# Kernel optimization log

Hardware: AMD Instinct MI355X
Metric: run time of the kernel (lower is better)

Reference implementation:

```python
import jax, jax.numpy as jnp
import numpy as np

NUM_HEADS = 16

def setup_inputs() -> dict:
    key = jax.random.key(0)
    ks = jax.random.split(key, 5)
    B, T, C = 2, 2048, 1024
    s = 0.02
    return {
        "x": jax.random.normal(ks[0], (B, T, C), dtype=jnp.float32),
        "attn_w": jax.random.normal(ks[1], (3 * C, C), dtype=jnp.float32) * s,
        "attn_b": jax.random.normal(ks[2], (3 * C,), dtype=jnp.float32) * s,
        "proj_w": jax.random.normal(ks[3], (C, C), dtype=jnp.float32) * s,
        "proj_b": jax.random.normal(ks[4], (C,), dtype=jnp.float32) * s,
    }

def reference(x, attn_w, attn_b, proj_w, proj_b):
    B, T, C = x.shape
    H = NUM_HEADS
    D = C // H
    # fused QKV projection (torch Linear: x @ W^T + b)
    qkv = x @ attn_w.T + attn_b                      # [B, T, 3C]
    q, k, v = jnp.split(qkv, 3, axis=-1)             # each [B, T, C]
    # split heads -> [B, H, T, D]
    def heads(t):
        return t.reshape(B, T, H, D).transpose(0, 2, 1, 3)
    q, k, v = heads(q), heads(k), heads(v)
    scale = 1.0 / jnp.sqrt(jnp.asarray(D, dtype=x.dtype))
    scores = jnp.einsum("bhtd,bhsd->bhts", q, k) * scale   # [B, H, T, T]
    causal = jnp.tril(jnp.ones((T, T), dtype=bool))
    scores = jnp.where(causal[None, None], scores, jnp.asarray(-jnp.inf, dtype=scores.dtype))
    att = jax.nn.softmax(scores, axis=-1)
    out = jnp.einsum("bhts,bhsd->bhtd", att, v)      # [B, H, T, D]
    out = out.transpose(0, 2, 1, 3).reshape(B, T, C)
    return out @ proj_w.T + proj_b
```

## Files before the change

kernel.cpp:

```cpp
#include <hip/hip_runtime.h>
#include <hip/hip_bf16.h>

typedef __bf16 bf16_t;
typedef __bf16 bf16x4 __attribute__((ext_vector_type(4)));
typedef __bf16 bf16x8 __attribute__((ext_vector_type(8)));
typedef float f32x4 __attribute__((ext_vector_type(4)));
typedef float f32x8 __attribute__((ext_vector_type(8)));

#define MFMA16(a, b, c) __builtin_amdgcn_mfma_f32_16x16x32_bf16(a, b, c, 0, 0, 0)

#define GLOAD_LDS16(g, l)                                              \
  __builtin_amdgcn_global_load_lds(                                    \
      (const __attribute__((address_space(1))) unsigned int*)(g),      \
      (__attribute__((address_space(3))) unsigned int*)(l), 16, 0, 0)

constexpr int B = 2, T = 2048, C = 1024, H = 16, D = 64;
constexpr int NQKV = 3 * C;
constexpr int M = B * T;

#define QSCALE 0.18033688011112042f

struct LoOn  { static constexpr bool value = true;  };
struct LoOff { static constexpr bool value = false; };

__global__ __launch_bounds__(256) void cvt_kernel(
    const float* __restrict__ s0, bf16_t* __restrict__ d0, int n0,
    const float* __restrict__ s1, bf16_t* __restrict__ d1, int n1,
    const float* __restrict__ s2, bf16_t* __restrict__ d2, int n2)
{
  const float* s; bf16_t* d; int n;
  if (blockIdx.y == 0)      { s = s0; d = d0; n = n0; }
  else if (blockIdx.y == 1) { s = s1; d = d1; n = n1; }
  else                      { s = s2; d = d2; n = n2; }
  const int idx = (blockIdx.x * 256 + threadIdx.x) * 8;
  if (idx >= n) return;
  f32x8 t = *(const f32x8*)(s + idx);
  bf16x8 r;
#pragma unroll
  for (int j = 0; j < 8; ++j) r[j] = (bf16_t)t[j];
  *(bf16x8*)(d + idx) = r;
}

template<int BM, int BN, int MI, int NI>
__device__ __forceinline__ void gemm_mainloop_db(
    const bf16_t* __restrict__ A, const bf16_t* __restrict__ Wt,
    const int K, const int m0, const int n0,
    bf16_t* ldsA0, bf16_t* ldsA1, bf16_t* ldsB0, bf16_t* ldsB1,
    f32x4 acc[MI][NI])
{
  const int tid  = threadIdx.x;
  const int wv   = tid >> 6;
  const int lane = tid & 63;
  const int col  = lane & 15;
  const int quad = lane >> 4;
  const int lr8  = lane >> 3;
  const int cpos = lane & 7;
  const int wm = wv >> 1, wn = wv & 1;
  constexpr int AJ = BM / 32;
  constexpr int ARW = BM / 4;
  constexpr int BJ = BN / 32;
  constexpr int BRW = BN / 4;

  const bf16_t* ag[AJ]; const bf16_t* bg[BJ];
#pragma unroll
  for (int j = 0; j < AJ; ++j)
    ag[j] = A + (size_t)(m0 + wv * ARW + j * 8 + lr8) * K + (cpos ^ lr8) * 8;
#pragma unroll
  for (int j = 0; j < BJ; ++j)
    bg[j] = Wt + (size_t)(n0 + wv * BRW + j * 8 + lr8) * K + (cpos ^ lr8) * 8;

  const int xa = quad ^ (col & 7);
  const int niter = K / 64;

#pragma unroll
  for (int j = 0; j < AJ; ++j)
    GLOAD_LDS16(ag[j], ldsA0 + (wv * ARW + j * 8) * 64);
#pragma unroll
  for (int j = 0; j < BJ; ++j)
    GLOAD_LDS16(bg[j], ldsB0 + (wv * BRW + j * 8) * 64);

  for (int it = 0; it < niter; ++it) {
    __syncthreads();
    const bf16_t* cA = (it & 1) ? ldsA1 : ldsA0;
    const bf16_t* cB = (it & 1) ? ldsB1 : ldsB0;
    if (it + 1 < niter) {
      bf16_t* nA = (it & 1) ? ldsA0 : ldsA1;
      bf16_t* nB = (it & 1) ? ldsB0 : ldsB1;
      const int off = (it + 1) * 64;
#pragma unroll
      for (int j = 0; j < AJ; ++j)
        GLOAD_LDS16(ag[j] + off, nA + (wv * ARW + j * 8) * 64);
#pragma unroll
      for (int j = 0; j < BJ; ++j)
        GLOAD_LDS16(bg[j] + off, nB + (wv * BRW + j * 8) * 64);
    }
#pragma unroll
    for (int ks = 0; ks < 2; ++ks) {
      const int xk = (xa ^ (ks * 4)) * 8;
      bf16x8 af[MI], bfr[NI];
#pragma unroll
      for (int mi = 0; mi < MI; ++mi)
        af[mi] = *(const bf16x8*)(cA + (wm * (MI * 16) + mi * 16 + col) * 64 + xk);
#pragma unroll
      for (int ni = 0; ni < NI; ++ni)
        bfr[ni] = *(const bf16x8*)(cB + (wn * (NI * 16) + ni * 16 + col) * 64 + xk);
#pragma unroll
      for (int mi = 0; mi < MI; ++mi)
#pragma unroll
        for (int ni = 0; ni < NI; ++ni)
          acc[mi][ni] = MFMA16(af[mi], bfr[ni], acc[mi][ni]);
    }
  }
}

__global__ __launch_bounds__(256) void qkv_gemm_kernel(
    const bf16_t* __restrict__ x, const bf16_t* __restrict__ w,
    const float* __restrict__ bias,
    bf16_t* __restrict__ qws, bf16_t* __restrict__ kws, bf16_t* __restrict__ vws)
{
  __shared__ __align__(16) bf16_t ldsA[2][128 * 64];
  __shared__ __align__(16) bf16_t ldsB[2][128 * 64];
  const int lane = threadIdx.x & 63;
  const int wv   = threadIdx.x >> 6;
  const int col  = lane & 15;
  const int quad = lane >> 4;
  const int wm = wv >> 1, wn = wv & 1;
  const int m0 = blockIdx.y * 128;
  const int n0 = blockIdx.x * 128;

  f32x4 acc[4][4] = {};
  gemm_mainloop_db<128, 128, 4, 4>(x, w, C, m0, n0,
                                   ldsA[0], ldsA[1], ldsB[0], ldsB[1], acc);

  const int which = n0 >> 10;

  if (which == 2) {
    __syncthreads();
    bf16_t* vt = &ldsA[0][0] + wv * 4096;

#pragma unroll
    for (int ni = 0; ni < 4; ++ni) {
      const int n = n0 + wn * 64 + ni * 16 + col;
      const float bval = bias[n];
      const int dl = ni * 16 + col;
#pragma unroll
      for (int r = 0; r < 4; ++r) {
        bf16x4 pw;
#pragma unroll
        for (int mi = 0; mi < 4; ++mi)
          pw[mi] = (bf16_t)(acc[mi][ni][r] + bval);
        const int k = 2 * quad + (r >> 1);
        const int S = dl * 8 + (k ^ (dl & 7));
        *(bf16x4*)(vt + S * 8 + (r & 1) * 4) = pw;
      }
    }

    const int b   = (m0 + wm * 64) >> 11;
    const int t0w = (m0 + wm * 64) & (T - 1);
    const int h   = ((n0 + wn * 64) & (C - 1)) >> 6;
    const size_t bh = (size_t)(b * H + h);
    const int lr8 = lane >> 3;
    const int c8  = lane & 7;
#pragma unroll
    for (int j = 0; j < 8; ++j) {
      const int dl = j * 8 + lr8;
      const int d  = dl;
      bf16x8 row = *(const bf16x8*)(vt + (dl * 8 + (c8 ^ (dl & 7))) * 8);
      *(bf16x8*)(vws + (bh * D + d) * T + t0w + c8 * 8) = row;
    }
  } else {
#pragma unroll
    for (int ni = 0; ni < 4; ++ni) {
      const int n = n0 + wn * 64 + ni * 16 + col;
      const float bval = bias[n];
      const int c = n & (C - 1);
      const int h = c >> 6;
      const int d = c & 63;
#pragma unroll
      for (int mi = 0; mi < 4; ++mi) {
#pragma unroll
        for (int r = 0; r < 4; ++r) {
          const int m = m0 + wm * 64 + mi * 16 + quad * 4 + r;
          const int b = m >> 11;
          const int t = m & (T - 1);
          const size_t bh = (size_t)(b * H + h);
          if (which == 0)
            qws[(bh * T + t) * D + d] = (bf16_t)((acc[mi][ni][r] + bval) * QSCALE);
          else
            kws[(bh * T + t) * D + d] = (bf16_t)(acc[mi][ni][r] + bval);
        }
      }
    }
  }
}

__global__ __launch_bounds__(256) void attn_kernel(
    const bf16_t* __restrict__ qws, const bf16_t* __restrict__ kws,
    const bf16_t* __restrict__ vws, bf16_t* __restrict__ yws)
{
  const int id = blockIdx.x;
  const int bh = id & 31;
  const int pr = id >> 5;
  const int tid  = threadIdx.x;
  const int wv   = tid >> 6;
  const int lane = tid & 63;
  const int col  = lane & 15;
  const int quad = lane >> 4;

  const bf16_t* Q  = qws + (size_t)bh * T * D;
  const bf16_t* K  = kws + (size_t)bh * T * D;
  const bf16_t* Vt = vws + (size_t)bh * D * T;

  __shared__ __align__(16) bf16_t ldsK[2][64 * 64];
  __shared__ __align__(16) bf16_t ldsV[2][64 * 64];
  __shared__ __align__(16) bf16_t ldsPh_s[4][16 * 64];
  __shared__ __align__(16) bf16_t ldsPl_s[4][16 * 64];
  bf16_t* ldsPh = ldsPh_s[wv];
  bf16_t* ldsPl = ldsPl_s[wv];

  const int xs   = col & 7;
  const int cxq  = (quad ^ xs) * 8;
  const int lr8  = lane >> 3;
  const int ksrc = (lane & 7) ^ lr8;
  const int pxor = (quad & 1) * 4;
  const int b = bh >> 4;
  const int h = bh & 15;

  const int qt_h = 31 - pr, qt_l = pr;
  const int t0h = qt_h * 64, t0l = qt_l * 64;
  const int twh = t0h + 16 * wv, twl = t0l + 16 * wv;

  bf16x8 qfh0 = *(const bf16x8*)(Q + (size_t)(twh + col) * D + quad * 8);
  bf16x8 qfh1 = *(const bf16x8*)(Q + (size_t)(twh + col) * D + 32 + quad * 8);
  bf16x8 qfl0 = *(const bf16x8*)(Q + (size_t)(twl + col) * D + quad * 8);
  bf16x8 qfl1 = *(const bf16x8*)(Q + (size_t)(twl + col) * D + 32 + quad * 8);

  f32x4 oh[4] = {}, ol[4] = {};
  f32x4 lph = {}, lpl = {};

  auto stage = [&](int it) {
    const int sn = it * 64;
    bf16_t* dK = ldsK[it & 1];
    bf16_t* dV = ldsV[it & 1];
#pragma unroll
    for (int j = 0; j < 2; ++j) {
      GLOAD_LDS16(K + (size_t)(sn + 16 * wv + j * 8 + lr8) * D + ksrc * 8,
                  dK + (16 * wv + j * 8) * 64);
      GLOAD_LDS16(Vt + (size_t)(16 * wv + j * 8 + lr8) * T + sn + ksrc * 8,
                  dV + (16 * wv + j * 8) * 64);
    }
  };

  auto body = [&](auto LOC, const bf16_t* bK, const bf16_t* bV,
                  int s0, bool hdiag, bool ldiag) {
    constexpr bool LO = decltype(LOC)::value;
    f32x4 sch[4], scl[4];
    __builtin_amdgcn_s_setprio(1);
#pragma unroll
    for (int kb = 0; kb < 4; ++kb) {
      const bf16_t* kr = bK + (kb * 16 + col) * 64;
      bf16x8 kf0 = *(const bf16x8*)(kr + cxq);
      bf16x8 kf1 = *(const bf16x8*)(kr + (cxq ^ 32));
      f32x4 a = {};
      a = MFMA16(qfh0, kf0, a);
      a = MFMA16(qfh1, kf1, a);
      sch[kb] = a;
      if constexpr (LO) {
        f32x4 c = {};
        c = MFMA16(qfl0, kf0, c);
        c = MFMA16(qfl1, kf1, c);
        scl[kb] = c;
      }
    }
    __builtin_amdgcn_s_setprio(0);
#pragma unroll
    for (int r = 0; r < 4; ++r) {
      const int prow = (quad * 4 + r) * 64;
      const int pxr  = pxor + r;
      const int poff = prow + (((col >> 1) ^ pxr) * 8) + (col & 1) * 4;
      bf16x4 pw;
#pragma unroll
      for (int kb = 0; kb < 4; ++kb) {
        float p = __builtin_amdgcn_exp2f(sch[kb][r]);
        if (hdiag && (s0 + kb * 16 + col > twh + quad * 4 + r)) p = 0.0f;
        lph[r] += p;
        pw[kb] = (bf16_t)p;
      }
      *(bf16x4*)(ldsPh + poff) = pw;
      if constexpr (LO) {
        bf16x4 pl;
#pragma unroll
        for (int kb = 0; kb < 4; ++kb) {
          float p = __builtin_amdgcn_exp2f(scl[kb][r]);
          if (ldiag && (s0 + kb * 16 + col > twl + quad * 4 + r)) p = 0.0f;
          lpl[r] += p;
          pl[kb] = (bf16_t)p;
        }
        *(bf16x4*)(ldsPl + poff) = pl;
      }
    }
    __builtin_amdgcn_s_setprio(1);
#pragma unroll
    for (int ks = 0; ks < 2; ++ks) {
      const int xk = cxq ^ (ks * 32);
      bf16x8 pah = *(const bf16x8*)(ldsPh + col * 64 + xk);
      bf16x8 pal{};
      if constexpr (LO) pal = *(const bf16x8*)(ldsPl + col * 64 + xk);
#pragma unroll
      for (int ni = 0; ni < 4; ++ni) {
        bf16x8 vf = *(const bf16x8*)(bV + (ni * 16 + col) * 64 + xk);
        oh[ni] = MFMA16(pah, vf, oh[ni]);
        if constexpr (LO) ol[ni] = MFMA16(pal, vf, ol[ni]);
      }
    }
    __builtin_amdgcn_s_setprio(0);
  };

  stage(0);

  for (int it = 0; it < qt_l; ++it) {
    __syncthreads();
    stage(it + 1);
    body(LoOn{}, ldsK[it & 1], ldsV[it & 1], it * 64, false, false);
  }
  {
    const int it = qt_l;
    __syncthreads();
    stage(it + 1);
    body(LoOn{}, ldsK[it & 1], ldsV[it & 1], it * 64, false, true);
  }
  for (int it = qt_l + 1; it < qt_h; ++it) {
    __syncthreads();
    stage(it + 1);
    body(LoOff{}, ldsK[it & 1], ldsV[it & 1], it * 64, false, false);
  }
  {
    __syncthreads();
    body(LoOff{}, ldsK[qt_h & 1], ldsV[qt_h & 1], qt_h * 64, true, false);
  }

#pragma unroll
  for (int r = 0; r < 4; ++r) {
    float l0 = lph[r], l1 = lpl[r];
#pragma unroll
    for (int off = 1; off < 16; off <<= 1) {
      l0 += __shfl_xor(l0, off);
      l1 += __shfl_xor(l1, off);
    }
    const float rl0 = 1.0f / l0, rl1 = 1.0f / l1;
    const int th = twh + quad * 4 + r;
    const int tl = twl + quad * 4 + r;
#pragma unroll
    for (int ni = 0; ni < 4; ++ni) {
      const int d = ni * 16 + col;
      yws[((size_t)(b * T + th)) * C + h * D + d] = (bf16_t)(oh[ni][r] * rl0);
      yws[((size_t)(b * T + tl)) * C + h * D + d] = (bf16_t)(ol[ni][r] * rl1);
    }
  }
}

__global__ __launch_bounds__(256) void proj_gemm_kernel(
    const bf16_t* __restrict__ y, const bf16_t* __restrict__ w,
    const float* __restrict__ bias, float* __restrict__ out)
{
  __shared__ __align__(16) bf16_t ldsA[2][128 * 64];
  __shared__ __align__(16) bf16_t ldsB[2][64 * 64];
  const int lane = threadIdx.x & 63;
  const int wv   = threadIdx.x >> 6;
  const int col  = lane & 15;
  const int quad = lane >> 4;
  const int wm = wv >> 1, wn = wv & 1;
  const int m0 = blockIdx.y * 128;
  const int n0 = blockIdx.x * 64;

  f32x4 acc[4][2] = {};
  gemm_mainloop_db<128, 64, 4, 2>(y, w, C, m0, n0,
                                  ldsA[0], ldsA[1], ldsB[0], ldsB[1], acc);

#pragma unroll
  for (int ni = 0; ni < 2; ++ni) {
    const int n = n0 + wn * 32 + ni * 16 + col;
    const float bval = bias[n];
#pragma unroll
    for (int mi = 0; mi < 4; ++mi) {
#pragma unroll
      for (int r = 0; r < 4; ++r) {
        const int m = m0 + wm * 64 + mi * 16 + quad * 4 + r;
        out[(size_t)m * C + n] = acc[mi][ni][r] + bval;
      }
    }
  }
}

extern "C" void kernel_launch(void* const* d_in, const int* in_sizes, int n_in,
                              void* d_out, int out_size, void* d_ws, size_t ws_size,
                              hipStream_t stream) {
  const float* x      = (const float*)d_in[0];
  const float* attn_w = (const float*)d_in[1];
  const float* attn_b = (const float*)d_in[2];
  const float* proj_w = (const float*)d_in[3];
  const float* proj_b = (const float*)d_in[4];
  float* out = (float*)d_out;

  const size_t E = (size_t)B * H * T * D;
  char* ws = (char*)d_ws;
  bf16_t* qws = (bf16_t*)(ws);
  bf16_t* kws = (bf16_t*)(ws + 2 * E);
  bf16_t* vws = (bf16_t*)(ws + 4 * E);
  bf16_t* yws = (bf16_t*)(ws + 6 * E);
  bf16_t* xb  = (bf16_t*)(ws + 8 * E);
  bf16_t* awb = (bf16_t*)(ws + 10 * E);
  bf16_t* pwb = (bf16_t*)(ws + 11 * E + E / 2);

  const int NX = M * C, NAW = NQKV * C, NPW = C * C;
  cvt_kernel<<<dim3(NX / 2048, 3), 256, 0, stream>>>(
      x, xb, NX, attn_w, awb, NAW, proj_w, pwb, NPW);
  qkv_gemm_kernel<<<dim3(NQKV / 128, M / 128), 256, 0, stream>>>(
      xb, awb, attn_b, qws, kws, vws);
  attn_kernel<<<512, 256, 0, stream>>>(qws, kws, vws, yws);
  proj_gemm_kernel<<<dim3(C / 64, M / 128), 256, 0, stream>>>(
      yws, pwb, proj_b, out);
}
```

Measured before the change: 163.5 us.

## Switch GEMM mainloops from double- to single-buffered LDS to raise occupancy

```diff
diff --git a/kernel.cpp b/kernel.cpp
--- a/kernel.cpp
+++ b/kernel.cpp
@@ -42,10 +42,10 @@
 }
 
 template<int BM, int BN, int MI, int NI>
-__device__ __forceinline__ void gemm_mainloop_db(
+__device__ __forceinline__ void gemm_mainloop_sb(
     const bf16_t* __restrict__ A, const bf16_t* __restrict__ Wt,
     const int K, const int m0, const int n0,
-    bf16_t* ldsA0, bf16_t* ldsA1, bf16_t* ldsB0, bf16_t* ldsB1,
+    bf16_t* ldsA, bf16_t* ldsB,
     f32x4 acc[MI][NI])
 {
   const int tid  = threadIdx.x;
@@ -74,41 +74,38 @@
 
 #pragma unroll
   for (int j = 0; j < AJ; ++j)
-    GLOAD_LDS16(ag[j], ldsA0 + (wv * ARW + j * 8) * 64);
+    GLOAD_LDS16(ag[j], ldsA + (wv * ARW + j * 8) * 64);
 #pragma unroll
   for (int j = 0; j < BJ; ++j)
-    GLOAD_LDS16(bg[j], ldsB0 + (wv * BRW + j * 8) * 64);
+    GLOAD_LDS16(bg[j], ldsB + (wv * BRW + j * 8) * 64);
 
   for (int it = 0; it < niter; ++it) {
     __syncthreads();
-    const bf16_t* cA = (it & 1) ? ldsA1 : ldsA0;
-    const bf16_t* cB = (it & 1) ? ldsB1 : ldsB0;
-    if (it + 1 < niter) {
-      bf16_t* nA = (it & 1) ? ldsA0 : ldsA1;
-      bf16_t* nB = (it & 1) ? ldsB0 : ldsB1;
-      const int off = (it + 1) * 64;
-#pragma unroll
-      for (int j = 0; j < AJ; ++j)
-        GLOAD_LDS16(ag[j] + off, nA + (wv * ARW + j * 8) * 64);
-#pragma unroll
-      for (int j = 0; j < BJ; ++j)
-        GLOAD_LDS16(bg[j] + off, nB + (wv * BRW + j * 8) * 64);
-    }
 #pragma unroll
     for (int ks = 0; ks < 2; ++ks) {
       const int xk = (xa ^ (ks * 4)) * 8;
       bf16x8 af[MI], bfr[NI];
 #pragma unroll
       for (int mi = 0; mi < MI; ++mi)
-        af[mi] = *(const bf16x8*)(cA + (wm * (MI * 16) + mi * 16 + col) * 64 + xk);
+        af[mi] = *(const bf16x8*)(ldsA + (wm * (MI * 16) + mi * 16 + col) * 64 + xk);
 #pragma unroll
       for (int ni = 0; ni < NI; ++ni)
-        bfr[ni] = *(const bf16x8*)(cB + (wn * (NI * 16) + ni * 16 + col) * 64 + xk);
+        bfr[ni] = *(const bf16x8*)(ldsB + (wn * (NI * 16) + ni * 16 + col) * 64 + xk);
 #pragma unroll
       for (int mi = 0; mi < MI; ++mi)
 #pragma unroll
         for (int ni = 0; ni < NI; ++ni)
           acc[mi][ni] = MFMA16(af[mi], bfr[ni], acc[mi][ni]);
+    }
+    __syncthreads();
+    if (it + 1 < niter) {
+      const int off = (it + 1) * 64;
+#pragma unroll
+      for (int j = 0; j < AJ; ++j)
+        GLOAD_LDS16(ag[j] + off, ldsA + (wv * ARW + j * 8) * 64);
+#pragma unroll
+      for (int j = 0; j < BJ; ++j)
+        GLOAD_LDS16(bg[j] + off, ldsB + (wv * BRW + j * 8) * 64);
     }
   }
 }
@@ -118,8 +115,9 @@
     const float* __restrict__ bias,
     bf16_t* __restrict__ qws, bf16_t* __restrict__ kws, bf16_t* __restrict__ vws)
 {
-  __shared__ __align__(16) bf16_t ldsA[2][128 * 64];
-  __shared__ __align__(16) bf16_t ldsB[2][128 * 64];
+  __shared__ __align__(16) bf16_t ldsAB[2 * 128 * 64];
+  bf16_t* ldsA = ldsAB;
+  bf16_t* ldsB = ldsAB + 128 * 64;
   const int lane = threadIdx.x & 63;
   const int wv   = threadIdx.x >> 6;
   const int col  = lane & 15;
@@ -129,14 +127,13 @@
   const int n0 = blockIdx.x * 128;
 
   f32x4 acc[4][4] = {};
-  gemm_mainloop_db<128, 128, 4, 4>(x, w, C, m0, n0,
-                                   ldsA[0], ldsA[1], ldsB[0], ldsB[1], acc);
+  gemm_mainloop_sb<128, 128, 4, 4>(x, w, C, m0, n0, ldsA, ldsB, acc);
 
   const int which = n0 >> 10;
 
   if (which == 2) {
     __syncthreads();
-    bf16_t* vt = &ldsA[0][0] + wv * 4096;
+    bf16_t* vt = ldsAB + wv * 4096;
 
 #pragma unroll
     for (int ni = 0; ni < 4; ++ni) {
@@ -161,6 +158,7 @@
     const size_t bh = (size_t)(b * H + h);
     const int lr8 = lane >> 3;
     const int c8  = lane & 7;
+    __syncthreads();
 #pragma unroll
     for (int j = 0; j < 8; ++j) {
       const int dl = j * 8 + lr8;
@@ -363,8 +361,8 @@
     const bf16_t* __restrict__ y, const bf16_t* __restrict__ w,
     const float* __restrict__ bias, float* __restrict__ out)
 {
-  __shared__ __align__(16) bf16_t ldsA[2][128 * 64];
-  __shared__ __align__(16) bf16_t ldsB[2][64 * 64];
+  __shared__ __align__(16) bf16_t ldsA[128 * 64];
+  __shared__ __align__(16) bf16_t ldsB[64 * 64];
   const int lane = threadIdx.x & 63;
   const int wv   = threadIdx.x >> 6;
   const int col  = lane & 15;
@@ -374,8 +372,7 @@
   const int n0 = blockIdx.x * 64;
 
   f32x4 acc[4][2] = {};
-  gemm_mainloop_db<128, 64, 4, 2>(y, w, C, m0, n0,
-                                  ldsA[0], ldsA[1], ldsB[0], ldsB[1], acc);
+  gemm_mainloop_sb<128, 64, 4, 2>(y, w, C, m0, n0, ldsA, ldsB, acc);
 
 #pragma unroll
   for (int ni = 0; ni < 2; ++ni) {
```

Result: slower. 170.9 us (+4.5%).
